# Kernel tuning notes

Measured on AMD Instinct MI355X. Metric: run time of the kernel, lower is better.

## Reference

```python
import jax, jax.numpy as jnp
import numpy as np

NUM_HEADS = 4
LN_EPS = 1e-5


def rotate_half(x):
    x1 = x[..., ::2]
    x2 = x[..., 1::2]
    return jnp.stack((-x2, x1), axis=-1).reshape(x.shape)


def apply_rope(freqs, t):
    # freqs: [2, B, 1, S, hd] (cos, sin); t: [B, H, S, hd]
    return t * freqs[0] + rotate_half(t) * freqs[1]


def normalize_kpts(kpts):
    size = 1.0 + kpts.max(-2) - kpts.min(-2)          # [B, 2]
    shift = size / 2.0
    scale = size.max(-1) / 2.0                         # [B]
    return (kpts - shift[..., None, :]) / scale[..., None, None]


def posenc(kpts, Wr):
    proj = kpts @ Wr                                   # [B, S, hd//2]
    emb = jnp.stack([jnp.cos(proj), jnp.sin(proj)], 0)[:, :, None, :, :]  # [2,B,1,S,hd//2]
    return jnp.repeat(emb, 2, axis=-1)                 # [2, B, 1, S, hd]


def layer_norm(x, g, b):
    mu = x.mean(-1, keepdims=True)
    var = ((x - mu) ** 2).mean(-1, keepdims=True)
    return (x - mu) / jnp.sqrt(var + LN_EPS) * g + b


def ffn(x, W1, b1, g, bt, W2, b2):
    return jax.nn.gelu(layer_norm(x @ W1 + b1, g, bt), approximate=False) @ W2 + b2


def heads_split(t, H):  # [B,S,D] -> [B,H,S,hd]
    B, S, D = t.shape
    return t.reshape(B, S, H, D // H).transpose(0, 2, 1, 3)


def heads_merge(t):  # [B,H,S,hd] -> [B,S,D]
    B, H, S, hd = t.shape
    return t.transpose(0, 2, 1, 3).reshape(B, S, H * hd)


def self_block(x, enc, Wqkv, bqkv, Wo, bo, W1, b1, g, bt, W2, b2):
    B, S, D = x.shape
    H = NUM_HEADS
    hd = D // H
    qkv = (x @ Wqkv + bqkv).reshape(B, S, H, hd, 3).transpose(0, 2, 1, 3, 4)
    q, k, v = qkv[..., 0], qkv[..., 1], qkv[..., 2]
    q = apply_rope(enc, q)
    k = apply_rope(enc, k)
    sim = jnp.einsum('bhid,bhjd->bhij', q, k) * (hd ** -0.5)
    ctx = jnp.einsum('bhij,bhjd->bhid', jax.nn.softmax(sim, axis=-1), v)
    msg = heads_merge(ctx) @ Wo + bo
    return x + ffn(jnp.concatenate([x, msg], axis=-1), W1, b1, g, bt, W2, b2)


def cross_block(x0, x1, Wqk, bqk, Wv, bv, Wo, bo, W1, b1, g, bt, W2, b2):
    H = NUM_HEADS
    hd = x0.shape[-1] // H
    qk0 = heads_split(x0 @ Wqk + bqk, H)
    qk1 = heads_split(x1 @ Wqk + bqk, H)
    v0 = heads_split(x0 @ Wv + bv, H)
    v1 = heads_split(x1 @ Wv + bv, H)
    sc = hd ** -0.25  # scale**0.5 applied to each of qk0, qk1
    sim = jnp.einsum('bhid,bhjd->bhij', qk0 * sc, qk1 * sc)
    m0 = jnp.einsum('bhij,bhjd->bhid', jax.nn.softmax(sim, axis=-1), v1)
    m1 = jnp.einsum('bhij,bhid->bhjd', jax.nn.softmax(sim, axis=-2), v0)
    m0 = heads_merge(m0) @ Wo + bo
    m1 = heads_merge(m1) @ Wo + bo
    x0 = x0 + ffn(jnp.concatenate([x0, m0], axis=-1), W1, b1, g, bt, W2, b2)
    x1 = x1 + ffn(jnp.concatenate([x1, m1], axis=-1), W1, b1, g, bt, W2, b2)
    return x0, x1


def setup_inputs() -> dict:
    key = jax.random.key(0)
    ks = iter(jax.random.split(key, 64))
    B, M, N, D, L = 2, 1024, 1024, 256, 9
    hd = D // NUM_HEADS
    def nrm(shape, scale):
        return jax.random.normal(next(ks), shape, jnp.float32) * scale
    s = 1.0 / np.sqrt(D)
    s2 = 1.0 / np.sqrt(2 * D)
    return {
        'kpts0': jax.random.uniform(next(ks), (B, M, 2), jnp.float32) * 1024.0,
        'kpts1': jax.random.uniform(next(ks), (B, N, 2), jnp.float32) * 1024.0,
        'desc0': nrm((B, M, D), 1.0),
        'desc1': nrm((B, N, D), 1.0),
        'Wr': nrm((2, hd // 2), 1.0),
        'Win': nrm((D, D), s), 'b_in': jnp.zeros(D),
        'sWqkv': nrm((L, D, 3 * D), s), 'sbqkv': jnp.zeros((L, 3 * D)),
        'sWo': nrm((L, D, D), s), 'sbo': jnp.zeros((L, D)),
        'sW1': nrm((L, 2 * D, 2 * D), s2), 'sb1': jnp.zeros((L, 2 * D)),
        'sg': jnp.ones((L, 2 * D)), 'sbt': jnp.zeros((L, 2 * D)),
        'sW2': nrm((L, 2 * D, D), s2), 'sb2': jnp.zeros((L, D)),
        'cWqk': nrm((L, D, D), s), 'cbqk': jnp.zeros((L, D)),
        'cWv': nrm((L, D, D), s), 'cbv': jnp.zeros((L, D)),
        'cWo': nrm((L, D, D), s), 'cbo': jnp.zeros((L, D)),
        'cW1': nrm((L, 2 * D, 2 * D), s2), 'cb1': jnp.zeros((L, 2 * D)),
        'cg': jnp.ones((L, 2 * D)), 'cbt': jnp.zeros((L, 2 * D)),
        'cW2': nrm((L, 2 * D, D), s2), 'cb2': jnp.zeros((L, D)),
        'Wf': nrm((D, D), s), 'bf': jnp.zeros(D),
        'Wlv': nrm((D, 2), s), 'blv': jnp.zeros(2),
    }


def reference(kpts0, kpts1, desc0, desc1, Wr, Win, b_in,
              sWqkv, sbqkv, sWo, sbo, sW1, sb1, sg, sbt, sW2, sb2,
              cWqk, cbqk, cWv, cbv, cWo, cbo, cW1, cb1, cg, cbt, cW2, cb2,
              Wf, bf, Wlv, blv):
    enc0 = posenc(normalize_kpts(kpts0), Wr)
    enc1 = posenc(normalize_kpts(kpts1), Wr)
    x0 = desc0 @ Win + b_in
    x1 = desc1 @ Win + b_in
    for l in range(sWqkv.shape[0]):
        x0 = self_block(x0, enc0, sWqkv[l], sbqkv[l], sWo[l], sbo[l],
                        sW1[l], sb1[l], sg[l], sbt[l], sW2[l], sb2[l])
        x1 = self_block(x1, enc1, sWqkv[l], sbqkv[l], sWo[l], sbo[l],
                        sW1[l], sb1[l], sg[l], sbt[l], sW2[l], sb2[l])
        x0, x1 = cross_block(x0, x1, cWqk[l], cbqk[l], cWv[l], cbv[l], cWo[l], cbo[l],
                             cW1[l], cb1[l], cg[l], cbt[l], cW2[l], cb2[l])
    d = x0.shape[-1]
    md0 = (x0 @ Wf + bf) / d ** 0.25
    md1 = (x1 @ Wf + bf) / d ** 0.25
    sim = jnp.einsum('bmd,bnd->bmn', md0, md1)
    p_rp_01 = jax.nn.softmax(sim, axis=-1)
    p_rp_10 = jax.nn.softmax(sim, axis=-2)  # == softmax(sim^T, -1)^T
    logvar_01 = x0 @ Wlv + blv
    logvar_10 = x1 @ Wlv + blv
    return (p_rp_01, p_rp_10, logvar_01, logvar_10)
```

## Files before the change

### kernel.cpp

```cpp
#include <hip/hip_runtime.h>
#include <hip/hip_bf16.h>
#include <math.h>

using bf16 = __hip_bfloat16;
typedef __attribute__((ext_vector_type(8))) short short8;
typedef __attribute__((ext_vector_type(4))) float f32x4;

#define LOG2E 1.44269504f

__device__ __forceinline__ float bf2f(bf16 x){ return __bfloat162float(x); }
__device__ __forceinline__ bf16  f2bf(float x){ return __float2bfloat16(x); }
__device__ __forceinline__ float ldin(const void* p, size_t i, int f){
  return f ? ((const float*)p)[i] : bf2f(((const bf16*)p)[i]);
}
__device__ __forceinline__ void stout(void* out, size_t i, float v, int f){
  if (f) ((float*)out)[i] = v; else ((bf16*)out)[i] = f2bf(v);
}
__device__ __forceinline__ void split2(float v, bf16* hi, bf16* lo){
  bf16 h = f2bf(v); *hi = h; *lo = f2bf(v - bf2f(h));
}
#define MFMA(a, b, c) __builtin_amdgcn_mfma_f32_16x16x32_bf16(a, b, c, 0, 0, 0)

__global__ void sniff_kernel(const unsigned* __restrict__ sg, int* __restrict__ flag)
{
  if (threadIdx.x == 0 && blockIdx.x == 0) *flag = (sg[0] == 0x3F800000u) ? 1 : 0;
}

__global__ __launch_bounds__(256) void cvtf_kernel(const void* __restrict__ src, float* __restrict__ dst,
                                                   int n, int chunk, int ldd, int doff,
                                                   const int* __restrict__ flag)
{
  int f = *flag;
  int i = blockIdx.x * 256 + threadIdx.x;
  if (i < n) dst[(size_t)(i / chunk) * ldd + doff + (i % chunk)] = ldin(src, i, f);
}

__global__ __launch_bounds__(256) void splitin_kernel(const void* __restrict__ src,
                                                      bf16* __restrict__ hi, bf16* __restrict__ lo,
                                                      int n, const int* __restrict__ flag)
{
  int f = *flag;
  int i = blockIdx.x * 256 + threadIdx.x;
  if (i < n) split2(ldin(src, i, f), &hi[i], &lo[i]);
}

template<bool ADDC>
__global__ __launch_bounds__(256) void gemm2_kernel(
    const bf16* __restrict__ Ahi, const bf16* __restrict__ Alo,
    const bf16* __restrict__ Bhi, const bf16* __restrict__ Blo,
    float* __restrict__ C, bf16* __restrict__ Chi, bf16* __restrict__ Clo,
    const float* __restrict__ bias,
    int K, int lda, int ldb, int ldc, int ldcp,
    long sAb, long sBb, long sCb, float scale)
{
  int z = blockIdx.z;
  Ahi += (size_t)z * sAb; Alo += (size_t)z * sAb;
  Bhi += (size_t)z * sBb; Blo += (size_t)z * sBb;
  size_t coff = (size_t)z * sCb;
  const int bm = blockIdx.y * 64, bn = blockIdx.x * 64;
  __shared__ bf16 AsH[64][72], AsL[64][72], BsH[64][72], BsL[64][72];
  const int tid  = threadIdx.x;
  const int lane = tid & 63, wid = tid >> 6;
  const int wr = wid >> 1, wc = wid & 1;
  const int srow = tid >> 2, sch = (tid & 3) * 8;
  const int lr = lane & 15, kg = (lane >> 4) * 8;
  f32x4 zero = {0.f, 0.f, 0.f, 0.f};
  f32x4 acc[2][2] = {{zero, zero}, {zero, zero}};
  for (int kt = 0; kt < K; kt += 64) {
    __syncthreads();
    size_t arow = (size_t)(bm + srow) * lda + kt + sch;
    size_t brow = (size_t)(bn + srow) * ldb + kt + sch;
    *(short8*)&AsH[srow][sch]      = *(const short8*)&Ahi[arow];
    *(short8*)&AsH[srow][sch + 32] = *(const short8*)&Ahi[arow + 32];
    *(short8*)&AsL[srow][sch]      = *(const short8*)&Alo[arow];
    *(short8*)&AsL[srow][sch + 32] = *(const short8*)&Alo[arow + 32];
    *(short8*)&BsH[srow][sch]      = *(const short8*)&Bhi[brow];
    *(short8*)&BsH[srow][sch + 32] = *(const short8*)&Bhi[brow + 32];
    *(short8*)&BsL[srow][sch]      = *(const short8*)&Blo[brow];
    *(short8*)&BsL[srow][sch + 32] = *(const short8*)&Blo[brow + 32];
    __syncthreads();
    #pragma unroll
    for (int kk = 0; kk < 2; kk++) {
      int kc = kk * 32 + kg;
      short8 ah0 = *(const short8*)&AsH[wr * 32 + lr][kc];
      short8 ah1 = *(const short8*)&AsH[wr * 32 + 16 + lr][kc];
      short8 al0 = *(const short8*)&AsL[wr * 32 + lr][kc];
      short8 al1 = *(const short8*)&AsL[wr * 32 + 16 + lr][kc];
      short8 bh0 = *(const short8*)&BsH[wc * 32 + lr][kc];
      short8 bh1 = *(const short8*)&BsH[wc * 32 + 16 + lr][kc];
      short8 bl0 = *(const short8*)&BsL[wc * 32 + lr][kc];
      short8 bl1 = *(const short8*)&BsL[wc * 32 + 16 + lr][kc];
      acc[0][0] = MFMA(ah0, bh0, acc[0][0]);
      acc[0][1] = MFMA(ah0, bh1, acc[0][1]);
      acc[1][0] = MFMA(ah1, bh0, acc[1][0]);
      acc[1][1] = MFMA(ah1, bh1, acc[1][1]);
      acc[0][0] = MFMA(ah0, bl0, acc[0][0]);
      acc[0][1] = MFMA(ah0, bl1, acc[0][1]);
      acc[1][0] = MFMA(ah1, bl0, acc[1][0]);
      acc[1][1] = MFMA(ah1, bl1, acc[1][1]);
      acc[0][0] = MFMA(al0, bh0, acc[0][0]);
      acc[0][1] = MFMA(al0, bh1, acc[0][1]);
      acc[1][0] = MFMA(al1, bh0, acc[1][0]);
      acc[1][1] = MFMA(al1, bh1, acc[1][1]);
    }
  }
  #pragma unroll
  for (int i = 0; i < 2; i++)
    #pragma unroll
    for (int j = 0; j < 2; j++) {
      int col = bn + wc * 32 + j * 16 + lr;
      float bv = bias ? bias[col] : 0.f;
      #pragma unroll
      for (int r = 0; r < 4; r++) {
        int row = bm + wr * 32 + i * 16 + (lane >> 4) * 4 + r;
        float v = (acc[i][j][r] + bv) * scale;
        if (C) {
          size_t idx = coff + (size_t)row * ldc + col;
          if (ADDC) v += C[idx];
          C[idx] = v;
        }
        if (Chi) {
          size_t idxp = (size_t)row * ldcp + col;
          split2(v, &Chi[idxp], &Clo[idxp]);
        }
      }
    }
}

template<bool ADDC>
static void gemm2(hipStream_t st, const bf16* Ahi, const bf16* Alo, const bf16* Bhi, const bf16* Blo,
                  float* C, bf16* Chi, bf16* Clo, const float* bias,
                  int M, int N, int K, int lda, int ldb, int ldc, int ldcp,
                  int Z, long sAb, long sBb, long sCb, float scale)
{
  dim3 g(N / 64, M / 64, Z);
  gemm2_kernel<ADDC><<<g, 256, 0, st>>>(Ahi, Alo, Bhi, Blo, C, Chi, Clo, bias,
                                        K, lda, ldb, ldc, ldcp, sAb, sBb, sCb, scale);
}

__global__ __launch_bounds__(256) void fattn_kernel(
    const bf16* __restrict__ Qh, const bf16* __restrict__ Ql,
    const bf16* __restrict__ Kh, const bf16* __restrict__ Kl,
    const bf16* __restrict__ Vh, const bf16* __restrict__ Vl,
    float* __restrict__ pO, float* __restrict__ pm, float* __restrict__ pl,
    int ldq, int cross, float scale)
{
  const int S = 1024;
  int z = blockIdx.y, half = blockIdx.z;
  size_t qoff, koff, voff;
  if (!cross) {
    qoff = (size_t)z * S * 64; koff = qoff;
    voff = (size_t)z * 64 * S;
  } else {
    int dir = z >> 3, b = (z >> 2) & 1, h = z & 3;
    size_t off0 = (size_t)b * S * 512 + (size_t)h * 64;
    size_t off1 = (size_t)(2048 + b * 1024) * 512 + (size_t)h * 64;
    if (dir == 0) { qoff = off0; koff = off1; voff = (size_t)(8 + b * 4 + h) * 64 * S; }
    else          { qoff = off1; koff = off0; voff = (size_t)(b * 4 + h) * 64 * S; }
  }
  __shared__ bf16 KsH[64][72], KsL[64][72], VsH[64][72], VsL[64][72];
  __shared__ bf16 PsH[4][16][72], PsL[4][16][72];
  const int tid = threadIdx.x;
  const int lane = tid & 63, w = tid >> 6;
  const int lr = lane & 15, kg8 = (lane >> 4) * 8;
  const int q0 = blockIdx.x * 64;
  const float sl2 = scale * LOG2E;
  int qrow = q0 + (w << 4) + lr;
  short8 aQh[2], aQl[2];
  #pragma unroll
  for (int kk = 0; kk < 2; kk++) {
    size_t qi = qoff + (size_t)qrow * ldq + kk * 32 + kg8;
    aQh[kk] = *(const short8*)&Qh[qi];
    aQl[kk] = *(const short8*)&Ql[qi];
  }
  f32x4 zero = {0.f, 0.f, 0.f, 0.f};
  f32x4 accO[4] = {zero, zero, zero, zero};
  float m[4] = {-1e30f, -1e30f, -1e30f, -1e30f};
  float l[4] = {0.f, 0.f, 0.f, 0.f};
  const int srow = tid >> 2, sch = (tid & 3) * 8;
  for (int kt = half * 8; kt < half * 8 + 8; kt++) {
    __syncthreads();
    size_t ki = koff + (size_t)(kt * 64 + srow) * ldq + sch;
    size_t vi = voff + (size_t)srow * S + kt * 64 + sch;
    *(short8*)&KsH[srow][sch]      = *(const short8*)&Kh[ki];
    *(short8*)&KsH[srow][sch + 32] = *(const short8*)&Kh[ki + 32];
    *(short8*)&KsL[srow][sch]      = *(const short8*)&Kl[ki];
    *(short8*)&KsL[srow][sch + 32] = *(const short8*)&Kl[ki + 32];
    *(short8*)&VsH[srow][sch]      = *(const short8*)&Vh[vi];
    *(short8*)&VsH[srow][sch + 32] = *(const short8*)&Vh[vi + 32];
    *(short8*)&VsL[srow][sch]      = *(const short8*)&Vl[vi];
    *(short8*)&VsL[srow][sch + 32] = *(const short8*)&Vl[vi + 32];
    __syncthreads();
    f32x4 s[4] = {zero, zero, zero, zero};
    #pragma unroll
    for (int kk = 0; kk < 2; kk++)
      #pragma unroll
      for (int j = 0; j < 4; j++) {
        short8 bh = *(const short8*)&KsH[j * 16 + lr][kk * 32 + kg8];
        short8 bl = *(const short8*)&KsL[j * 16 + lr][kk * 32 + kg8];
        s[j] = MFMA(aQh[kk], bh, s[j]);
        s[j] = MFMA(aQh[kk], bl, s[j]);
        s[j] = MFMA(aQl[kk], bh, s[j]);
      }
    #pragma unroll
    for (int j = 0; j < 4; j++)
      #pragma unroll
      for (int r = 0; r < 4; r++) s[j][r] *= sl2;
    float fac[4], rs[4];
    #pragma unroll
    for (int r = 0; r < 4; r++) {
      float v = fmaxf(fmaxf(s[0][r], s[1][r]), fmaxf(s[2][r], s[3][r]));
      #pragma unroll
      for (int o = 8; o; o >>= 1) v = fmaxf(v, __shfl_xor(v, o));
      float nm = fmaxf(m[r], v);
      fac[r] = exp2f(m[r] - nm);
      m[r] = nm;
      rs[r] = 0.f;
    }
    #pragma unroll
    for (int j = 0; j < 4; j++)
      #pragma unroll
      for (int r = 0; r < 4; r++) {
        float p = exp2f(s[j][r] - m[r]);
        s[j][r] = p;
        rs[r] += p;
      }
    #pragma unroll
    for (int r = 0; r < 4; r++) {
      float v = rs[r];
      #pragma unroll
      for (int o = 8; o; o >>= 1) v += __shfl_xor(v, o);
      l[r] = l[r] * fac[r] + v;
      #pragma unroll
      for (int n = 0; n < 4; n++) accO[n][r] *= fac[r];
    }
    #pragma unroll
    for (int j = 0; j < 4; j++)
      #pragma unroll
      for (int r = 0; r < 4; r++)
        split2(s[j][r], &PsH[w][(lane >> 4) * 4 + r][j * 16 + lr],
                        &PsL[w][(lane >> 4) * 4 + r][j * 16 + lr]);
    #pragma unroll
    for (int kk = 0; kk < 2; kk++) {
      short8 pah = *(const short8*)&PsH[w][lr][kk * 32 + kg8];
      short8 pal = *(const short8*)&PsL[w][lr][kk * 32 + kg8];
      #pragma unroll
      for (int n = 0; n < 4; n++) {
        short8 vh = *(const short8*)&VsH[n * 16 + lr][kk * 32 + kg8];
        short8 vl = *(const short8*)&VsL[n * 16 + lr][kk * 32 + kg8];
        accO[n] = MFMA(pah, vh, accO[n]);
        accO[n] = MFMA(pah, vl, accO[n]);
        accO[n] = MFMA(pal, vh, accO[n]);
      }
    }
  }
  int hz = half * 16 + z;
  #pragma unroll
  for (int n = 0; n < 4; n++)
    #pragma unroll
    for (int r = 0; r < 4; r++) {
      int row = q0 + (w << 4) + (lane >> 4) * 4 + r;
      pO[((size_t)hz * 1024 + row) * 64 + n * 16 + lr] = accO[n][r];
    }
  if (lr == 0) {
    #pragma unroll
    for (int r = 0; r < 4; r++) {
      int row = q0 + (w << 4) + (lane >> 4) * 4 + r;
      pm[(size_t)hz * 1024 + row] = m[r];
      pl[(size_t)hz * 1024 + row] = l[r];
    }
  }
}

__global__ __launch_bounds__(256) void fattn_combine_kernel(
    const float* __restrict__ pO, const float* __restrict__ pm, const float* __restrict__ pl,
    bf16* __restrict__ Oh, bf16* __restrict__ Ol, int cross)
{
  const int S = 1024;
  int idx = blockIdx.x * 256 + threadIdx.x;
  int col = idx & 63;
  int row = (idx >> 6) & 1023;
  int z = idx >> 16;
  size_t r0 = (size_t)z * 1024 + row, r1 = r0 + 16 * 1024;
  float m0 = pm[r0], m1 = pm[r1];
  float M = fmaxf(m0, m1);
  float e0 = exp2f(m0 - M), e1 = exp2f(m1 - M);
  float den = pl[r0] * e0 + pl[r1] * e1;
  float v = (pO[r0 * 64 + col] * e0 + pO[r1 * 64 + col] * e1) / den;
  size_t ooff;
  if (!cross) ooff = (size_t)(z >> 2) * S * 256 + (size_t)(z & 3) * 64;
  else {
    int dir = z >> 3, b = (z >> 2) & 1, h = z & 3;
    ooff = dir == 0 ? (size_t)b * S * 256 + (size_t)h * 64
                    : (size_t)(2048 + b * 1024) * 256 + (size_t)h * 64;
  }
  size_t oi = ooff + (size_t)row * 256 + col;
  split2(v, &Oh[oi], &Ol[oi]);
}

__global__ __launch_bounds__(256) void transpose2_kernel(const void* __restrict__ src,
                                                         bf16* __restrict__ dhi, bf16* __restrict__ dlo,
                                                         int R, int C, long sDstZ, long dOff,
                                                         const int* __restrict__ flag)
{
  __shared__ float tile[32][33];
  int f = *flag;
  size_t zsrc = (size_t)blockIdx.z * R * C;
  size_t zdst = (size_t)blockIdx.z * sDstZ + dOff;
  int c0 = blockIdx.x * 32, r0 = blockIdx.y * 32;
  int x = threadIdx.x, y = threadIdx.y;
  for (int i = y; i < 32; i += 8)
    tile[i][x] = ldin(src, zsrc + (size_t)(r0 + i) * C + (c0 + x), f);
  __syncthreads();
  for (int i = y; i < 32; i += 8) {
    size_t di = zdst + (size_t)(c0 + i) * R + (r0 + x);
    split2(tile[x][i], &dhi[di], &dlo[di]);
  }
}

__global__ __launch_bounds__(256) void minmax_kernel(const void* __restrict__ k0,
                                                     const void* __restrict__ k1,
                                                     float* __restrict__ mm, const int* __restrict__ flag)
{
  int f = *flag;
  int z = blockIdx.x;
  const void* kp = (z >= 2) ? k1 : k0;
  size_t base = (size_t)(z & 1) * 1024 * 2;
  int t = threadIdx.x;
  float mnx = 1e30f, mxx = -1e30f, mny = 1e30f, mxy = -1e30f;
  for (int s = t; s < 1024; s += 256) {
    float x = ldin(kp, base + s * 2, f), y = ldin(kp, base + s * 2 + 1, f);
    mnx = fminf(mnx, x); mxx = fmaxf(mxx, x);
    mny = fminf(mny, y); mxy = fmaxf(mxy, y);
  }
  for (int o = 32; o; o >>= 1) {
    mnx = fminf(mnx, __shfl_xor(mnx, o)); mxx = fmaxf(mxx, __shfl_xor(mxx, o));
    mny = fminf(mny, __shfl_xor(mny, o)); mxy = fmaxf(mxy, __shfl_xor(mxy, o));
  }
  __shared__ float r[4][4];
  if ((t & 63) == 0) { int w = t >> 6; r[w][0] = mnx; r[w][1] = mxx; r[w][2] = mny; r[w][3] = mxy; }
  __syncthreads();
  if (t == 0) {
    for (int w = 1; w < 4; w++) {
      r[0][0] = fminf(r[0][0], r[w][0]); r[0][1] = fmaxf(r[0][1], r[w][1]);
      r[0][2] = fminf(r[0][2], r[w][2]); r[0][3] = fmaxf(r[0][3], r[w][3]);
    }
    mm[z * 4 + 0] = r[0][0]; mm[z * 4 + 1] = r[0][1]; mm[z * 4 + 2] = r[0][2]; mm[z * 4 + 3] = r[0][3];
  }
}

__global__ __launch_bounds__(256) void posenc_kernel(const void* __restrict__ k0, const void* __restrict__ k1,
                                                     const float* __restrict__ mm, const void* __restrict__ Wr,
                                                     float* __restrict__ ecos, float* __restrict__ esin,
                                                     const int* __restrict__ flag)
{
  int f = *flag;
  int idx = blockIdx.x * 256 + threadIdx.x;
  int z = idx >> 10;
  const void* kp = (z >= 2) ? k1 : k0;
  size_t base = (size_t)(z & 1) * 1024 * 2 + (size_t)(idx & 1023) * 2;
  float sx = 1.f + mm[z * 4 + 1] - mm[z * 4 + 0];
  float sy = 1.f + mm[z * 4 + 3] - mm[z * 4 + 2];
  float scale = fmaxf(sx, sy) * 0.5f;
  float xn = (ldin(kp, base, f)     - sx * 0.5f) / scale;
  float yn = (ldin(kp, base + 1, f) - sy * 0.5f) / scale;
  for (int j = 0; j < 32; j++) {
    float p = xn * ldin(Wr, j, f) + yn * ldin(Wr, 32 + j, f);
    ecos[(size_t)idx * 32 + j] = cosf(p);
    esin[(size_t)idx * 32 + j] = sinf(p);
  }
}

__global__ __launch_bounds__(256) void rope_kernel(const float* __restrict__ qkv,
                                                   const float* __restrict__ ecos, const float* __restrict__ esin,
                                                   bf16* __restrict__ qh, bf16* __restrict__ ql,
                                                   bf16* __restrict__ kh, bf16* __restrict__ kl,
                                                   bf16* __restrict__ vh, bf16* __restrict__ vl)
{
  int idx = blockIdx.x * 256 + threadIdx.x;
  int row = idx >> 5, p = idx & 31;
  int zz = row >> 10, s = row & 1023;
  float c  = ecos[(size_t)row * 32 + p];
  float sn = esin[(size_t)row * 32 + p];
  const float* qp = qkv + (size_t)row * 768;
  #pragma unroll
  for (int h = 0; h < 4; h++) {
    int base = h * 192 + p * 6;
    float q0 = qp[base + 0], k0 = qp[base + 1], v0 = qp[base + 2];
    float q1 = qp[base + 3], k1 = qp[base + 4], v1 = qp[base + 5];
    int zh = zz * 4 + h;
    size_t qo = ((size_t)zh * 1024 + s) * 64 + 2 * p;
    split2(q0 * c - q1 * sn, &qh[qo],     &ql[qo]);
    split2(q1 * c + q0 * sn, &qh[qo + 1], &ql[qo + 1]);
    split2(k0 * c - k1 * sn, &kh[qo],     &kl[qo]);
    split2(k1 * c + k0 * sn, &kh[qo + 1], &kl[qo + 1]);
    size_t vo = ((size_t)zh * 64 + 2 * p) * 1024 + s;
    split2(v0, &vh[vo],        &vl[vo]);
    split2(v1, &vh[vo + 1024], &vl[vo + 1024]);
  }
}

__global__ __launch_bounds__(256) void vsplitT_kernel(const bf16* __restrict__ vhi, const bf16* __restrict__ vlo,
                                                      bf16* __restrict__ vThi, bf16* __restrict__ vTlo, int ld)
{
  __shared__ bf16 tile[32][33];
  int zz = blockIdx.z >> 1, plane = blockIdx.z & 1;
  const bf16* v  = plane ? vlo  : vhi;
  bf16*       vT = plane ? vTlo : vThi;
  int h = blockIdx.y >> 1, d0 = (blockIdx.y & 1) * 32;
  int s0 = blockIdx.x * 32;
  int x = threadIdx.x, y = threadIdx.y;
  const bf16* sp = v + ((size_t)zz * 1024 + s0) * ld + h * 64 + d0;
  for (int i = y; i < 32; i += 8) tile[i][x] = sp[(size_t)i * ld + x];
  __syncthreads();
  bf16* dp = vT + (((size_t)(zz * 4 + h)) * 64 + d0) * 1024 + s0;
  for (int i = y; i < 32; i += 8) dp[(size_t)i * 1024 + x] = tile[x][i];
}

__global__ __launch_bounds__(256) void row_softmax_kernel(const float* __restrict__ in,
                                                          void* __restrict__ outp, size_t eoff,
                                                          const int* __restrict__ flagp)
{
  int f = *flagp;
  size_t row = blockIdx.x;
  const float* ip = in + row * 1024;
  int t = threadIdx.x;
  float v[4]; float mx = -1e30f;
  #pragma unroll
  for (int i = 0; i < 4; i++) { v[i] = ip[t + i * 256] * LOG2E; mx = fmaxf(mx, v[i]); }
  #pragma unroll
  for (int o = 32; o; o >>= 1) mx = fmaxf(mx, __shfl_xor(mx, o));
  __shared__ float red[4];
  if ((t & 63) == 0) red[t >> 6] = mx;
  __syncthreads();
  mx = fmaxf(fmaxf(red[0], red[1]), fmaxf(red[2], red[3]));
  float sm = 0.f;
  #pragma unroll
  for (int i = 0; i < 4; i++) { v[i] = exp2f(v[i] - mx); sm += v[i]; }
  #pragma unroll
  for (int o = 32; o; o >>= 1) sm += __shfl_xor(sm, o);
  __shared__ float red2[4];
  if ((t & 63) == 0) red2[t >> 6] = sm;
  __syncthreads();
  sm = red2[0] + red2[1] + red2[2] + red2[3];
  float inv = 1.f / sm;
  size_t ob = eoff + row * 1024;
  #pragma unroll
  for (int i = 0; i < 4; i++) stout(outp, ob + t + i * 256, v[i] * inv, f);
}

__global__ __launch_bounds__(256) void col_softmax_kernel(const float* __restrict__ sim, void* __restrict__ out,
                                                          size_t eoff, const int* __restrict__ flagp)
{
  int f = *flagp;
  int b = blockIdx.y;
  int tid = threadIdx.x;
  int lane = tid & 63, w = tid >> 6;
  int lc = tid & 15;
  int g  = tid >> 4;
  int c = blockIdx.x * 16 + lc;
  const float* sp = sim + (size_t)b * 1048576 + c;
  float mx = -1e30f;
  for (int r = g; r < 1024; r += 16) mx = fmaxf(mx, sp[(size_t)r * 1024]);
  mx = fmaxf(mx, __shfl_xor(mx, 16));
  mx = fmaxf(mx, __shfl_xor(mx, 32));
  __shared__ float redm[4][16], reds[4][16];
  if ((lane >> 4) == 0) redm[w][lc] = mx;
  __syncthreads();
  mx = fmaxf(fmaxf(redm[0][lc], redm[1][lc]), fmaxf(redm[2][lc], redm[3][lc]));
  mx *= LOG2E;
  float sm = 0.f;
  for (int r = g; r < 1024; r += 16) sm += exp2f(sp[(size_t)r * 1024] * LOG2E - mx);
  sm += __shfl_xor(sm, 16);
  sm += __shfl_xor(sm, 32);
  if ((lane >> 4) == 0) reds[w][lc] = sm;
  __syncthreads();
  sm = reds[0][lc] + reds[1][lc] + reds[2][lc] + reds[3][lc];
  float inv = 1.f / sm;
  size_t ob = eoff + (size_t)b * 1048576 + c;
  for (int r = g; r < 1024; r += 16)
    stout(out, ob + (size_t)r * 1024, exp2f(sp[(size_t)r * 1024] * LOG2E - mx) * inv, f);
}

__global__ __launch_bounds__(256) void ln_gelu_kernel(const bf16* __restrict__ hh, const bf16* __restrict__ hl,
                                                      bf16* __restrict__ oh, bf16* __restrict__ ol,
                                                      const float* __restrict__ g, const float* __restrict__ bt)
{
  size_t row = blockIdx.x;
  const bf16 *hp = hh + row * 512, *lp = hl + row * 512;
  int t = threadIdx.x;
  float a = bf2f(hp[t]) + bf2f(lp[t]);
  float b = bf2f(hp[t + 256]) + bf2f(lp[t + 256]);
  float s = a + b, s2 = a * a + b * b;
  #pragma unroll
  for (int o = 32; o; o >>= 1) { s += __shfl_xor(s, o); s2 += __shfl_xor(s2, o); }
  __shared__ float r1[4], r2[4];
  if ((t & 63) == 0) { r1[t >> 6] = s; r2[t >> 6] = s2; }
  __syncthreads();
  s = r1[0] + r1[1] + r1[2] + r1[3];
  s2 = r2[0] + r2[1] + r2[2] + r2[3];
  float mu = s * (1.f / 512.f);
  float var = s2 * (1.f / 512.f) - mu * mu;
  float inv = rsqrtf(var + 1e-5f);
  float o1 = (a - mu) * inv * g[t] + bt[t];
  float o2 = (b - mu) * inv * g[t + 256] + bt[t + 256];
  o1 = 0.5f * o1 * (1.f + erff(o1 * 0.70710678118f));
  o2 = 0.5f * o2 * (1.f + erff(o2 * 0.70710678118f));
  split2(o1, &oh[row * 512 + t],       &ol[row * 512 + t]);
  split2(o2, &oh[row * 512 + t + 256], &ol[row * 512 + t + 256]);
}

__global__ __launch_bounds__(256) void logvar_kernel(const float* __restrict__ x, const void* __restrict__ Wlv,
                                                     const void* __restrict__ blv, void* __restrict__ out,
                                                     size_t eoff, const int* __restrict__ flagp)
{
  int f = *flagp;
  int idx = blockIdx.x * 256 + threadIdx.x;
  int r = idx >> 1, c = idx & 1;
  float acc = ldin(blv, c, f);
  const float* xp = x + (size_t)r * 256;
  for (int d = 0; d < 256; d++) acc += xp[d] * ldin(Wlv, d * 2 + c, f);
  int img = r >> 11, rs = r & 2047;
  stout(out, eoff + (size_t)img * 4096 + rs * 2 + c, acc, f);
}

extern "C" void kernel_launch(void* const* d_in, const int* in_sizes, int n_in,
                              void* d_out, int out_size, void* d_ws, size_t ws_size,
                              hipStream_t stream)
{
  (void)in_sizes; (void)n_in; (void)out_size; (void)ws_size;
  const int L = 9, S = 1024;
  const long SS = (long)S * S;
  char* w = (char*)d_ws; size_t off = 0;
  auto alloc = [&](size_t bytes) -> void* {
    void* p = w + off; off = (off + bytes + 1023) & ~(size_t)1023; return p;
  };
  struct Pair { bf16 *hi, *lo; };
  auto apair = [&](size_t elems) -> Pair {
    Pair p; p.hi = (bf16*)alloc(elems * 2); p.lo = (bf16*)alloc(elems * 2); return p;
  };
  int*   flag  = (int*)alloc(4);
  float* mm    = (float*)alloc(16 * 4);
  float* b_in  = (float*)alloc(256 * 4);
  float* sbqkv = (float*)alloc((size_t)L * 768 * 4);
  float* sbo   = (float*)alloc((size_t)L * 256 * 4);
  float* sb1   = (float*)alloc((size_t)L * 512 * 4);
  float* sg    = (float*)alloc((size_t)L * 512 * 4);
  float* sbt   = (float*)alloc((size_t)L * 512 * 4);
  float* sb2   = (float*)alloc((size_t)L * 256 * 4);
  float* cbqkv = (float*)alloc((size_t)L * 512 * 4);
  float* cbo   = (float*)alloc((size_t)L * 256 * 4);
  float* cb1   = (float*)alloc((size_t)L * 512 * 4);
  float* cg    = (float*)alloc((size_t)L * 512 * 4);
  float* cbt   = (float*)alloc((size_t)L * 512 * 4);
  float* cb2   = (float*)alloc((size_t)L * 256 * 4);
  float* bfv   = (float*)alloc(256 * 4);
  Pair WinT   = apair(65536);
  Pair WfT    = apair(65536);
  Pair sWqkvT = apair((size_t)L * 196608);
  Pair sWoT   = apair((size_t)L * 65536);
  Pair sW1T   = apair((size_t)L * 262144);
  Pair sW2T   = apair((size_t)L * 131072);
  Pair cWqkvT = apair((size_t)L * 131072);
  Pair cWoT   = apair((size_t)L * 65536);
  Pair cW1T   = apair((size_t)L * 262144);
  Pair cW2T   = apair((size_t)L * 131072);
  float* ecos  = (float*)alloc((size_t)4 * S * 32 * 4);
  float* esin  = (float*)alloc((size_t)4 * S * 32 * 4);
  float* xall  = (float*)alloc((size_t)4096 * 256 * 4);
  Pair qP      = apair((size_t)16 * S * 64);
  Pair kP      = apair((size_t)16 * S * 64);
  Pair vTP     = apair((size_t)16 * 64 * S);
  Pair catP    = apair((size_t)4096 * 512);
  Pair hmP     = apair((size_t)4096 * 512);
  Pair ctxP    = apair((size_t)4096 * 256);
  float* qkvb  = (float*)alloc((size_t)4096 * 768 * 4);
  float* pO    = (float*)alloc((size_t)2 * 16 * 1024 * 64 * 4);
  float* pm    = (float*)alloc((size_t)32 * 1024 * 4);
  float* pl    = (float*)alloc((size_t)32 * 1024 * 4);
  float* simf  = pO;
  bf16* XH = catP.hi;
  bf16* XL = catP.lo;
  Pair qkv2P = {(bf16*)qkvb, (bf16*)qkvb + (size_t)4096 * 512};
  Pair xinP  = {(bf16*)qkvb, (bf16*)qkvb + (size_t)4096 * 256};
  Pair mdP   = {(bf16*)qkvb, (bf16*)qkvb + (size_t)4096 * 256};

  sniff_kernel<<<1, 64, 0, stream>>>((const unsigned*)d_in[13], flag);

  auto cvtf = [&](const void* src, float* dst, int n) {
    cvtf_kernel<<<(n + 255) / 256, 256, 0, stream>>>(src, dst, n, n, n, 0, flag);
  };
  cvtf(d_in[6],  b_in,  256);
  cvtf(d_in[8],  sbqkv, L * 768);
  cvtf(d_in[10], sbo,   L * 256);
  cvtf(d_in[12], sb1,   L * 512);
  cvtf(d_in[13], sg,    L * 512);
  cvtf(d_in[14], sbt,   L * 512);
  cvtf(d_in[16], sb2,   L * 256);
  cvtf_kernel<<<(L * 256 + 255) / 256, 256, 0, stream>>>(d_in[18], cbqkv, L * 256, 256, 512, 0, flag);
  cvtf_kernel<<<(L * 256 + 255) / 256, 256, 0, stream>>>(d_in[20], cbqkv, L * 256, 256, 512, 256, flag);
  cvtf(d_in[22], cbo,   L * 256);
  cvtf(d_in[24], cb1,   L * 512);
  cvtf(d_in[25], cg,    L * 512);
  cvtf(d_in[26], cbt,   L * 512);
  cvtf(d_in[28], cb2,   L * 256);
  cvtf(d_in[30], bfv,   256);

  dim3 tb(32, 8);
  transpose2_kernel<<<dim3(8, 8, 1), tb, 0, stream>>>(d_in[5],  WinT.hi,   WinT.lo,   256, 256, 65536, 0, flag);
  transpose2_kernel<<<dim3(8, 8, 1), tb, 0, stream>>>(d_in[29], WfT.hi,    WfT.lo,    256, 256, 65536, 0, flag);
  transpose2_kernel<<<dim3(24, 8, L), tb, 0, stream>>>(d_in[7],  sWqkvT.hi, sWqkvT.lo, 256, 768, 196608, 0, flag);
  transpose2_kernel<<<dim3(8, 8, L), tb, 0, stream>>>(d_in[9],  sWoT.hi,   sWoT.lo,   256, 256, 65536, 0, flag);
  transpose2_kernel<<<dim3(16, 16, L), tb, 0, stream>>>(d_in[11], sW1T.hi,  sW1T.lo,  512, 512, 262144, 0, flag);
  transpose2_kernel<<<dim3(8, 16, L), tb, 0, stream>>>(d_in[15], sW2T.hi,   sW2T.lo,  512, 256, 131072, 0, flag);
  transpose2_kernel<<<dim3(8, 8, L), tb, 0, stream>>>(d_in[17], cWqkvT.hi, cWqkvT.lo, 256, 256, 131072, 0, flag);
  transpose2_kernel<<<dim3(8, 8, L), tb, 0, stream>>>(d_in[19], cWqkvT.hi, cWqkvT.lo, 256, 256, 131072, 65536, flag);
  transpose2_kernel<<<dim3(8, 8, L), tb, 0, stream>>>(d_in[21], cWoT.hi,   cWoT.lo,   256, 256, 65536, 0, flag);
  transpose2_kernel<<<dim3(16, 16, L), tb, 0, stream>>>(d_in[23], cW1T.hi,  cW1T.lo,  512, 512, 262144, 0, flag);
  transpose2_kernel<<<dim3(8, 16, L), tb, 0, stream>>>(d_in[27], cW2T.hi,   cW2T.lo,  512, 256, 131072, 0, flag);

  minmax_kernel<<<4, 256, 0, stream>>>(d_in[0], d_in[1], mm, flag);
  posenc_kernel<<<16, 256, 0, stream>>>(d_in[0], d_in[1], mm, d_in[4], ecos, esin, flag);

  splitin_kernel<<<2048, 256, 0, stream>>>(d_in[2], xinP.hi, xinP.lo, 2048 * 256, flag);
  splitin_kernel<<<2048, 256, 0, stream>>>(d_in[3], xinP.hi + (size_t)2048 * 256,
                                           xinP.lo + (size_t)2048 * 256, 2048 * 256, flag);
  gemm2<false>(stream, xinP.hi, xinP.lo, WinT.hi, WinT.lo, xall, XH, XL, b_in,
               4096, 256, 256, 256, 256, 256, 512, 1, 0, 0, 0, 1.f);

  for (int l = 0; l < L; l++) {
    gemm2<false>(stream, XH, XL, sWqkvT.hi + (size_t)l * 196608, sWqkvT.lo + (size_t)l * 196608,
                 qkvb, nullptr, nullptr, sbqkv + l * 768,
                 4096, 768, 256, 512, 256, 768, 0, 1, 0, 0, 0, 1.f);
    rope_kernel<<<512, 256, 0, stream>>>(qkvb, ecos, esin, qP.hi, qP.lo, kP.hi, kP.lo, vTP.hi, vTP.lo);
    fattn_kernel<<<dim3(16, 16, 2), 256, 0, stream>>>(qP.hi, qP.lo, kP.hi, kP.lo, vTP.hi, vTP.lo,
                                                      pO, pm, pl, 64, 0, 0.125f);
    fattn_combine_kernel<<<4096, 256, 0, stream>>>(pO, pm, pl, ctxP.hi, ctxP.lo, 0);
    gemm2<false>(stream, ctxP.hi, ctxP.lo, sWoT.hi + (size_t)l * 65536, sWoT.lo + (size_t)l * 65536,
                 nullptr, catP.hi + 256, catP.lo + 256, sbo + l * 256,
                 4096, 256, 256, 256, 256, 0, 512, 1, 0, 0, 0, 1.f);
    gemm2<false>(stream, catP.hi, catP.lo, sW1T.hi + (size_t)l * 262144, sW1T.lo + (size_t)l * 262144,
                 nullptr, hmP.hi, hmP.lo, sb1 + l * 512,
                 4096, 512, 512, 512, 512, 0, 512, 1, 0, 0, 0, 1.f);
    ln_gelu_kernel<<<4096, 256, 0, stream>>>(hmP.hi, hmP.lo, hmP.hi, hmP.lo, sg + l * 512, sbt + l * 512);
    gemm2<true>(stream, hmP.hi, hmP.lo, sW2T.hi + (size_t)l * 131072, sW2T.lo + (size_t)l * 131072,
                xall, XH, XL, sb2 + l * 256,
                4096, 256, 512, 512, 512, 256, 512, 1, 0, 0, 0, 1.f);

    gemm2<false>(stream, XH, XL, cWqkvT.hi + (size_t)l * 131072, cWqkvT.lo + (size_t)l * 131072,
                 nullptr, qkv2P.hi, qkv2P.lo, cbqkv + l * 512,
                 4096, 512, 256, 512, 256, 0, 512, 1, 0, 0, 0, 1.f);
    vsplitT_kernel<<<dim3(32, 8, 8), tb, 0, stream>>>(qkv2P.hi + 256, qkv2P.lo + 256, vTP.hi, vTP.lo, 512);
    fattn_kernel<<<dim3(16, 16, 2), 256, 0, stream>>>(qkv2P.hi, qkv2P.lo, qkv2P.hi, qkv2P.lo, vTP.hi, vTP.lo,
                                                      pO, pm, pl, 512, 1, 0.125f);
    fattn_combine_kernel<<<4096, 256, 0, stream>>>(pO, pm, pl, ctxP.hi, ctxP.lo, 1);
    gemm2<false>(stream, ctxP.hi, ctxP.lo, cWoT.hi + (size_t)l * 65536, cWoT.lo + (size_t)l * 65536,
                 nullptr, catP.hi + 256, catP.lo + 256, cbo + l * 256,
                 4096, 256, 256, 256, 256, 0, 512, 1, 0, 0, 0, 1.f);
    gemm2<false>(stream, catP.hi, catP.lo, cW1T.hi + (size_t)l * 262144, cW1T.lo + (size_t)l * 262144,
                 nullptr, hmP.hi, hmP.lo, cb1 + l * 512,
                 4096, 512, 512, 512, 512, 0, 512, 1, 0, 0, 0, 1.f);
    ln_gelu_kernel<<<4096, 256, 0, stream>>>(hmP.hi, hmP.lo, hmP.hi, hmP.lo, cg + l * 512, cbt + l * 512);
    gemm2<true>(stream, hmP.hi, hmP.lo, cW2T.hi + (size_t)l * 131072, cW2T.lo + (size_t)l * 131072,
                xall, XH, XL, cb2 + l * 256,
                4096, 256, 512, 512, 512, 256, 512, 1, 0, 0, 0, 1.f);
  }

  gemm2<false>(stream, XH, XL, WfT.hi, WfT.lo, nullptr, mdP.hi, mdP.lo, bfv,
               4096, 256, 256, 512, 256, 0, 256, 1, 0, 0, 0, 0.25f);
  gemm2<false>(stream, mdP.hi, mdP.lo, mdP.hi + (size_t)2048 * 256, mdP.lo + (size_t)2048 * 256,
               simf, nullptr, nullptr, nullptr,
               1024, 1024, 256, 256, 256, 1024, 0, 2, (long)1024 * 256, (long)1024 * 256, SS, 1.f);
  row_softmax_kernel<<<2048, 256, 0, stream>>>(simf, d_out, 0, flag);
  col_softmax_kernel<<<dim3(64, 2), 256, 0, stream>>>(simf, d_out, 2097152, flag);
  logvar_kernel<<<32, 256, 0, stream>>>(xall, d_in[31], d_in[32], d_out, 4194304, flag);
}
```

Measured before the change: 2.002 ms.

## Load GEMM tiles directly into LDS with XOR-swizzled layout

```diff
diff --git a/kernel.cpp b/kernel.cpp
--- a/kernel.cpp
+++ b/kernel.cpp
@@ -20,6 +20,8 @@
   bf16 h = f2bf(v); *hi = h; *lo = f2bf(v - bf2f(h));
 }
 #define MFMA(a, b, c) __builtin_amdgcn_mfma_f32_16x16x32_bf16(a, b, c, 0, 0, 0)
+#define LDSW(base, row, kc) (*(const short8*)((const char*)(base) + ((row) << 7) + \
+                              (((((kc) >> 3) ^ ((row) & 7))) << 4)))
 
 __global__ void sniff_kernel(const unsigned* __restrict__ sg, int* __restrict__ flag)
 {
@@ -58,38 +60,41 @@
   Bhi += (size_t)z * sBb; Blo += (size_t)z * sBb;
   size_t coff = (size_t)z * sCb;
   const int bm = blockIdx.y * 64, bn = blockIdx.x * 64;
-  __shared__ bf16 AsH[64][72], AsL[64][72], BsH[64][72], BsL[64][72];
+  __shared__ bf16 AsH[64][64], AsL[64][64], BsH[64][64], BsL[64][64];
   const int tid  = threadIdx.x;
-  const int lane = tid & 63, wid = tid >> 6;
-  const int wr = wid >> 1, wc = wid & 1;
-  const int srow = tid >> 2, sch = (tid & 3) * 8;
+  const int lane = tid & 63, w = tid >> 6;
+  const int wr = w >> 1, wc = w & 1;
   const int lr = lane & 15, kg = (lane >> 4) * 8;
+  const int srl = lane >> 3;
+  const int cg  = ((lane & 7) ^ srl) << 3;
   f32x4 zero = {0.f, 0.f, 0.f, 0.f};
   f32x4 acc[2][2] = {{zero, zero}, {zero, zero}};
   for (int kt = 0; kt < K; kt += 64) {
     __syncthreads();
-    size_t arow = (size_t)(bm + srow) * lda + kt + sch;
-    size_t brow = (size_t)(bn + srow) * ldb + kt + sch;
-    *(short8*)&AsH[srow][sch]      = *(const short8*)&Ahi[arow];
-    *(short8*)&AsH[srow][sch + 32] = *(const short8*)&Ahi[arow + 32];
-    *(short8*)&AsL[srow][sch]      = *(const short8*)&Alo[arow];
-    *(short8*)&AsL[srow][sch + 32] = *(const short8*)&Alo[arow + 32];
-    *(short8*)&BsH[srow][sch]      = *(const short8*)&Bhi[brow];
-    *(short8*)&BsH[srow][sch + 32] = *(const short8*)&Bhi[brow + 32];
-    *(short8*)&BsL[srow][sch]      = *(const short8*)&Blo[brow];
-    *(short8*)&BsL[srow][sch + 32] = *(const short8*)&Blo[brow + 32];
+    #pragma unroll
+    for (int j = 0; j < 2; j++) {
+      int r = (w << 4) + j * 8;
+      size_t ao = (size_t)(bm + r + srl) * lda + kt + cg;
+      size_t bo = (size_t)(bn + r + srl) * ldb + kt + cg;
+      __builtin_amdgcn_global_load_lds(&Ahi[ao], &AsH[r][0], 16, 0, 0);
+      __builtin_amdgcn_global_load_lds(&Alo[ao], &AsL[r][0], 16, 0, 0);
+      __builtin_amdgcn_global_load_lds(&Bhi[bo], &BsH[r][0], 16, 0, 0);
+      __builtin_amdgcn_global_load_lds(&Blo[bo], &BsL[r][0], 16, 0, 0);
+    }
     __syncthreads();
     #pragma unroll
     for (int kk = 0; kk < 2; kk++) {
       int kc = kk * 32 + kg;
-      short8 ah0 = *(const short8*)&AsH[wr * 32 + lr][kc];
-      short8 ah1 = *(const short8*)&AsH[wr * 32 + 16 + lr][kc];
-      short8 al0 = *(const short8*)&AsL[wr * 32 + lr][kc];
-      short8 al1 = *(const short8*)&AsL[wr * 32 + 16 + lr][kc];
-      short8 bh0 = *(const short8*)&BsH[wc * 32 + lr][kc];
-      short8 bh1 = *(const short8*)&BsH[wc * 32 + 16 + lr][kc];
-      short8 bl0 = *(const short8*)&BsL[wc * 32 + lr][kc];
-      short8 bl1 = *(const short8*)&BsL[wc * 32 + 16 + lr][kc];
+      int r0 = wr * 32 + lr, r1 = r0 + 16;
+      int c0 = wc * 32 + lr, c1 = c0 + 16;
+      short8 ah0 = LDSW(AsH, r0, kc);
+      short8 ah1 = LDSW(AsH, r1, kc);
+      short8 al0 = LDSW(AsL, r0, kc);
+      short8 al1 = LDSW(AsL, r1, kc);
+      short8 bh0 = LDSW(BsH, c0, kc);
+      short8 bh1 = LDSW(BsH, c1, kc);
+      short8 bl0 = LDSW(BsL, c0, kc);
+      short8 bl1 = LDSW(BsL, c1, kc);
       acc[0][0] = MFMA(ah0, bh0, acc[0][0]);
       acc[0][1] = MFMA(ah0, bh1, acc[0][1]);
       acc[1][0] = MFMA(ah1, bh0, acc[1][0]);
```

New measurement: 1.983 ms. Within noise of the previous version (-0.9%).
